# Optimization experiments

Measured on AMD Instinct MI355X. Metric: run time of the kernel, lower is better.

Reference implementation:

```python
import jax, jax.numpy as jnp
import numpy as np

P = 5.0  # p-norm order from init_kwargs


def setup_inputs() -> dict:
    key = jax.random.key(0)
    k1, k2 = jax.random.split(key)
    B, N, M, C = 8, 4096, 4096, 3
    x = jax.random.normal(k1, (B, N, C), dtype=jnp.float32)
    y = jax.random.normal(k2, (B, M, C), dtype=jnp.float32)
    return {"x": x, "y": y}


def _pnorm(v, axis):
    # (sum |v|^p)^(1/p), matching torch.norm(p=5)
    return jnp.sum(jnp.abs(v) ** P, axis=axis) ** (1.0 / P)


def reference(x, y):
    # Squared Euclidean distance matrix [B, N, M]
    d = (-2.0 * jnp.einsum("bnc,bmc->bnm", x, y)
         + jnp.sum(x * x, -1)[:, :, None]
         + jnp.sum(y * y, -1)[:, None, :])
    idx1 = jnp.argmin(d, axis=2)  # [B, N]: nearest y for each x
    idx2 = jnp.argmin(d, axis=1)  # [B, M]: nearest x for each y
    nn_y = jnp.take_along_axis(y, idx1[..., None], axis=1)  # [B, N, 3]
    nn_x = jnp.take_along_axis(x, idx2[..., None], axis=1)  # [B, M, 3]
    pc1 = _pnorm(x - nn_y, axis=-1)  # [B, N]
    pc2 = _pnorm(y - nn_x, axis=-1)  # [B, M]
    result2 = _pnorm(pc1, axis=-1) + _pnorm(pc2, axis=-1)  # [B]
    return jnp.mean(result2)
```

## Files before the change

kernel.cpp:

```cpp
#include <hip/hip_runtime.h>
#include <math.h>


#define BQ      256
#define QPT     2
#define SPLITS  16
#define CH      256
#define GS      8
#define NG      (CH / GS)
#define BIGOFF  64.0f
#define NQTOT   65536
#define NTILE   128
#define TILEQ   512

typedef float f32x2 __attribute__((ext_vector_type(2)));

static __device__ __forceinline__ f32x2 mk2(float s) { f32x2 v; v.x = s; v.y = s; return v; }
static __device__ __forceinline__ f32x2 fma2(f32x2 a, f32x2 b, f32x2 c) {
    return __builtin_elementwise_fma(a, b, c);
}
__device__ __forceinline__ unsigned int float_ord(float f) {
    unsigned int u = __float_as_uint(f);
    return (u & 0x80000000u) ? ~u : (u | 0x80000000u);
}

#define WS_ACC    0
#define WS_CANARY 128
#define WS_GCNT   192
#define WS_TCNT   256
#define WS_PSUM   1024
#define WS_TAB    4096
#define WS_TBL    1048576

__global__ __launch_bounds__(BQ) void chamfer_mktab(
    const float* __restrict__ x, const float* __restrict__ y,
    float4* __restrict__ tbl)
{
    const int t   = blockIdx.x * BQ + threadIdx.x;
    const int dir = t >> 14;
    const int b   = (t >> 11) & 7;
    const int pr  = t & 2047;
    const float* R = (dir == 0 ? y : x) + (size_t)b * 4096 * 3;
    const float* rp = R + (size_t)(2 * pr) * 3;
    const float f0 = rp[0], f1 = rp[1], f2 = rp[2];
    const float f3 = rp[3], f4 = rp[4], f5 = rp[5];
    const float h0 = fmaf(0.5f * f0, f0, fmaf(0.5f * f1, f1, fmaf(0.5f * f2, f2, BIGOFF)));
    const float h1 = fmaf(0.5f * f3, f3, fmaf(0.5f * f4, f4, fmaf(0.5f * f5, f5, BIGOFF)));
    const size_t o = ((size_t)(dir * 8 + b) * 2048 + pr) * 2;
    tbl[o]     = make_float4(f0, f3, f1, f4);
    tbl[o + 1] = make_float4(f2, f5, h0, h1);
}

__global__ __launch_bounds__(BQ, 8) void chamfer_fused_r12(
    const float* __restrict__ x, const float* __restrict__ y,
    const float4* __restrict__ tbl,
    unsigned long long* __restrict__ tab,
    unsigned int* __restrict__ tcnt, unsigned int* __restrict__ gcnt,
    const unsigned int* __restrict__ canary_p,
    float* __restrict__ psum, float* __restrict__ out)
{
    __shared__ float red[4];
    __shared__ int s_flag;

    const int bid   = blockIdx.x;
    const int split = bid & (SPLITS - 1);
    const int tq    = bid >> 4;
    const int dir   = tq >> 6;
    const int b     = (tq >> 3) & 7;
    const int t8    = tq & 7;

    const unsigned int canary = *canary_p;

    const float* Q; const float* R;
    if (dir == 0) { Q = x + (size_t)b * 4096 * 3; R = y + (size_t)b * 4096 * 3; }
    else          { Q = y + (size_t)b * 4096 * 3; R = x + (size_t)b * 4096 * 3; }

    const int tid = threadIdx.x;

    const float4* __restrict__ tb =
        tbl + ((size_t)(dir * 8 + b) * 4096 + (size_t)split * 256);

    const int ql0 = t8 * TILEQ + tid;
    const int ql1 = ql0 + 256;
    const float qx0 = Q[ql0 * 3 + 0], qy0 = Q[ql0 * 3 + 1], qz0 = Q[ql0 * 3 + 2];
    const float qx1 = Q[ql1 * 3 + 0], qy1 = Q[ql1 * 3 + 1], qz1 = Q[ql1 * 3 + 2];
    const f32x2 nqx0 = mk2(-qx0), nqy0 = mk2(-qy0), nqz0 = mk2(-qz0);
    const f32x2 nqx1 = mk2(-qx1), nqy1 = mk2(-qy1), nqz1 = mk2(-qz1);

    float best0 = 3.4e38f, best1 = 3.4e38f;
    int bg0 = 0, bg1 = 0;

    #pragma unroll 2
    for (int g = 0; g < NG; ++g) {
        float m0 = 3.4e38f, m1 = 3.4e38f;
        #pragma unroll
        for (int k = 0; k < GS / 2; ++k) {
            const float4 a = tb[(g * 4 + k) * 2];
            const float4 c = tb[(g * 4 + k) * 2 + 1];
            f32x2 rx; rx.x = a.x; rx.y = a.y;
            f32x2 ry; ry.x = a.z; ry.y = a.w;
            f32x2 rz; rz.x = c.x; rz.y = c.y;
            f32x2 h2; h2.x = c.z; h2.y = c.w;
            const f32x2 s0 = fma2(nqx0, rx, fma2(nqy0, ry, fma2(nqz0, rz, h2)));
            const f32x2 s1 = fma2(nqx1, rx, fma2(nqy1, ry, fma2(nqz1, rz, h2)));
            m0 = fminf(fminf(m0, s0.x), s0.y);
            m1 = fminf(fminf(m1, s1.x), s1.y);
        }
        const bool c0 = m0 < best0;
        best0 = c0 ? m0 : best0;  bg0 = c0 ? g : bg0;
        const bool c1 = m1 < best1;
        best1 = c1 ? m1 : best1;  bg1 = c1 ? g : bg1;
    }

    #pragma unroll
    for (int hh = 0; hh < 2; ++hh) {
        const float bscore = hh ? best1 : best0;
        const int   bg     = hh ? bg1   : bg0;
        const float qx = hh ? qx1 : qx0;
        const float qy = hh ? qy1 : qy0;
        const float qz = hh ? qz1 : qz0;
        const int basej = split * CH + bg * GS;
        int bj = basej;
        #pragma unroll
        for (int j = GS - 1; j >= 0; --j) {
            const float* rp = R + (size_t)(basej + j) * 3;
            const float rx = rp[0], ry = rp[1], rz = rp[2];
            const float h = fmaf(0.5f * rx, rx, fmaf(0.5f * ry, ry, fmaf(0.5f * rz, rz, BIGOFF)));
            const float s = fmaf(-qx, rx, fmaf(-qy, ry, fmaf(-qz, rz, h)));
            if (s == bscore) bj = basej + j;
        }
        const size_t qidx = (size_t)tq * TILEQ + hh * 256 + tid;
        const unsigned long long key =
            ~(((unsigned long long)__float_as_uint(bscore) << 32) | (unsigned int)bj);
        atomicMax(&tab[qidx], key);
    }

    __syncthreads();
    if (tid == 0) {
        const unsigned int old = atomicAdd(&tcnt[tq], 1u);
        s_flag = (old == canary + (SPLITS - 1));
    }
    __syncthreads();
    if (!s_flag) return;

    float sthr = 0.0f;
    #pragma unroll
    for (int k = 0; k < QPT; ++k) {
        const int gq = tq * TILEQ + k * 256 + tid;
        const int q  = t8 * TILEQ + k * 256 + tid;
        const unsigned long long w =
            ~__hip_atomic_load(&tab[gq], __ATOMIC_RELAXED, __HIP_MEMORY_SCOPE_AGENT);
        const int j = (int)(unsigned int)w;
        const float dx = Q[q * 3 + 0] - R[(size_t)j * 3 + 0];
        const float dy = Q[q * 3 + 1] - R[(size_t)j * 3 + 1];
        const float dz = Q[q * 3 + 2] - R[(size_t)j * 3 + 2];
        const float ax = fabsf(dx), ay = fabsf(dy), az = fabsf(dz);
        const float ax2 = ax * ax, ay2 = ay * ay, az2 = az * az;
        sthr += ax2 * ax2 * ax + ay2 * ay2 * ay + az2 * az2 * az;
    }
    #pragma unroll
    for (int off = 32; off > 0; off >>= 1) sthr += __shfl_down(sthr, off, 64);
    const int wid = tid >> 6, lane = tid & 63;
    if (lane == 0) red[wid] = sthr;
    __syncthreads();

    if (tid == 0) {
        __hip_atomic_store(&psum[tq], red[0] + red[1] + red[2] + red[3],
                           __ATOMIC_RELAXED, __HIP_MEMORY_SCOPE_AGENT);
        asm volatile("s_waitcnt vmcnt(0)" ::: "memory");
        const unsigned int old = atomicAdd(gcnt, 1u);
        s_flag = (old == canary + (NTILE - 1));
    }
    __syncthreads();
    if (!s_flag) return;

    if (tid < 64) {
        float v = 0.0f;
        if (tid < 16) {
            const int fb = tid >> 1, fdir = tid & 1;
            float a = 0.0f;
            #pragma unroll
            for (int t = 0; t < 8; ++t)
                a += __hip_atomic_load(&psum[fdir * 64 + fb * 8 + t],
                                       __ATOMIC_RELAXED, __HIP_MEMORY_SCOPE_AGENT);
            v = exp2f(0.2f * log2f(a));
        }
        #pragma unroll
        for (int off = 8; off > 0; off >>= 1) v += __shfl_down(v, off, 64);
        if (tid == 0) out[0] = v * 0.125f;
    }
    if (tid < NTILE)
        __hip_atomic_store(&tcnt[tid], canary, __ATOMIC_RELAXED, __HIP_MEMORY_SCOPE_AGENT);
    if (tid == 0)
        __hip_atomic_store(gcnt, canary, __ATOMIC_RELAXED, __HIP_MEMORY_SCOPE_AGENT);
}

__global__ __launch_bounds__(BQ) void chamfer_nn_split_kernel(
    const float* __restrict__ x, const float* __restrict__ y,
    unsigned long long* __restrict__ packed, int N, int M)
{
    __shared__ float4 sref[1024];
    const int bid = blockIdx.x, split = bid & 3, qb = bid >> 2;
    const int tile = qb & 15, dir = (qb >> 4) & 1, b = qb >> 5;
    const float* Q; const float* R;
    if (dir == 0) { Q = x + (size_t)b * N * 3; R = y + (size_t)b * M * 3; }
    else          { Q = y + (size_t)b * M * 3; R = x + (size_t)b * N * 3; }
    const int tid = threadIdx.x, q = tile * BQ + tid, base = split * 1024;
    for (int j = tid; j < 1024; j += BQ) {
        const float rx = R[(size_t)(base + j) * 3 + 0];
        const float ry = R[(size_t)(base + j) * 3 + 1];
        const float rz = R[(size_t)(base + j) * 3 + 2];
        sref[j] = make_float4(rx, ry, rz, 0.5f * (rx * rx + ry * ry + rz * rz));
    }
    __syncthreads();
    const float qx = Q[q * 3 + 0], qy = Q[q * 3 + 1], qz = Q[q * 3 + 2];
    float best = 3.4e38f; int bestj = base;
    #pragma unroll 8
    for (int j = 0; j < 1024; ++j) {
        const float4 r = sref[j];
        float t = __fmaf_rn(-qx, r.x, r.w);
        t = __fmaf_rn(-qy, r.y, t);
        t = __fmaf_rn(-qz, r.z, t);
        const bool c = t < best;
        best = c ? t : best; bestj = c ? (base + j) : bestj;
    }
    const size_t idx = ((size_t)dir * 8 + b) * (size_t)N + q;
    atomicMin(&packed[idx], ((unsigned long long)float_ord(best) << 32) | (unsigned int)bestj);
}

__global__ __launch_bounds__(BQ) void chamfer_gather_kernel(
    const float* __restrict__ x, const float* __restrict__ y,
    const unsigned long long* __restrict__ packed,
    float* __restrict__ acc, int N, int M)
{
    __shared__ float red[4];
    const int tid = threadIdx.x;
    const size_t gq = (size_t)blockIdx.x * BQ + tid;
    const int dir = (int)(gq / ((size_t)8 * N));
    const size_t rem = gq - (size_t)dir * 8 * N;
    const int b = (int)(rem / N), q = (int)(rem - (size_t)b * N);
    const float* Q; const float* R;
    if (dir == 0) { Q = x + (size_t)b * N * 3; R = y + (size_t)b * M * 3; }
    else          { Q = y + (size_t)b * M * 3; R = x + (size_t)b * N * 3; }
    const int j = (int)(unsigned int)packed[gq];
    const float dx = Q[q * 3 + 0] - R[(size_t)j * 3 + 0];
    const float dy = Q[q * 3 + 1] - R[(size_t)j * 3 + 1];
    const float dz = Q[q * 3 + 2] - R[(size_t)j * 3 + 2];
    const float ax = fabsf(dx), ay = fabsf(dy), az = fabsf(dz);
    const float ax2 = ax * ax, ay2 = ay * ay, az2 = az * az;
    float s = ax2 * ax2 * ax + ay2 * ay2 * ay + az2 * az2 * az;
    #pragma unroll
    for (int off = 32; off > 0; off >>= 1) s += __shfl_down(s, off, 64);
    const int wid = tid >> 6, lane = tid & 63;
    if (lane == 0) red[wid] = s;
    __syncthreads();
    if (tid == 0) atomicAdd(&acc[b * 2 + dir], red[0] + red[1] + red[2] + red[3]);
}

__global__ void chamfer_finalize_kernel(const float* __restrict__ acc,
                                        float* __restrict__ out)
{
    if (threadIdx.x == 0 && blockIdx.x == 0) {
        float total = 0.0f;
        #pragma unroll
        for (int i = 0; i < 16; ++i) total += powf(acc[i], 0.2f);
        *out = total * 0.125f;
    }
}

extern "C" void kernel_launch(void* const* d_in, const int* in_sizes, int n_in,
                              void* d_out, int out_size, void* d_ws, size_t ws_size,
                              hipStream_t stream)
{
    const float* x = (const float*)d_in[0];
    const float* y = (const float*)d_in[1];
    float* out = (float*)d_out;
    const int N = in_sizes[0] / 24;
    const int M = in_sizes[1] / 24;

    const size_t needed = WS_TBL + (size_t)32768 * 32;

    if (N == 4096 && M == 4096 && ws_size >= needed) {
        unsigned char* ws = (unsigned char*)d_ws;
        unsigned long long* tab = (unsigned long long*)(ws + WS_TAB);
        unsigned int* tcnt = (unsigned int*)(ws + WS_TCNT);
        unsigned int* gcnt = (unsigned int*)(ws + WS_GCNT);
        const unsigned int* canary = (const unsigned int*)(ws + WS_CANARY);
        float* psum = (float*)(ws + WS_PSUM);
        float4* tbl = (float4*)(ws + WS_TBL);
        chamfer_mktab<<<32768 / BQ, BQ, 0, stream>>>(x, y, tbl);
        chamfer_fused_r12<<<NTILE * SPLITS, BQ, 0, stream>>>(
            x, y, tbl, tab, tcnt, gcnt, canary, psum, out);
    } else {
        unsigned char* ws = (unsigned char*)d_ws;
        float* acc = (float*)ws;
        unsigned long long* ptab = (unsigned long long*)(ws + 4096);
        const size_t nQ = (size_t)2 * 8 * N;
        hipMemsetAsync(acc, 0, 64, stream);
        hipMemsetAsync(ptab, 0xFF, nQ * 8, stream);
        chamfer_nn_split_kernel<<<(int)(nQ / BQ) * 4, BQ, 0, stream>>>(x, y, ptab, N, M);
        chamfer_gather_kernel<<<(int)(nQ / BQ), BQ, 0, stream>>>(x, y, ptab, acc, N, M);
        chamfer_finalize_kernel<<<1, 64, 0, stream>>>(acc, out);
    }
}
```

Baseline: 89.82 us.

## Process four queries per thread and double-buffer reference table loads

Each thread now handles four query points instead of two, which halves the number of tiles and blocks so each loaded reference chunk is reused across more queries. The reference-table loads are software-pipelined with two register buffers, so the next group is fetched while the current one is computed. Launch bounds drop to 4 waves per SIMD to fit the extra registers, and the finalize indexing is adjusted for 64 tiles. The cost is higher register pressure and fewer blocks (1024), which lowers occupancy and parallelism.

```diff
diff --git a/kernel.cpp b/kernel.cpp
--- a/kernel.cpp
+++ b/kernel.cpp
@@ -3,17 +3,18 @@
 
 
 #define BQ      256
-#define QPT     2
+#define QPT     4
 #define SPLITS  16
 #define CH      256
 #define GS      8
 #define NG      (CH / GS)
 #define BIGOFF  64.0f
 #define NQTOT   65536
-#define NTILE   128
-#define TILEQ   512
+#define NTILE   64
+#define TILEQ   1024
 
 typedef float f32x2 __attribute__((ext_vector_type(2)));
+typedef float f32x4 __attribute__((ext_vector_type(4)));
 
 static __device__ __forceinline__ f32x2 mk2(float s) { f32x2 v; v.x = s; v.y = s; return v; }
 static __device__ __forceinline__ f32x2 fma2(f32x2 a, f32x2 b, f32x2 c) {
@@ -51,9 +52,36 @@
     tbl[o + 1] = make_float4(f2, f5, h0, h1);
 }
 
-__global__ __launch_bounds__(BQ, 8) void chamfer_fused_r12(
+#define COMPUTE_GROUP(BUF, G)                                              \
+  {                                                                        \
+    float mloc[QPT];                                                       \
+    _Pragma("unroll")                                                      \
+    for (int k4 = 0; k4 < 4; ++k4) {                                       \
+      const f32x4 a = BUF[2 * k4];                    \
+      const f32x4 c = BUF[2 * k4 + 1];                 \
+      const f32x2 rx = __builtin_shufflevector(a, a, 0, 1);                \
+      const f32x2 ry = __builtin_shufflevector(a, a, 2, 3);                \
+      const f32x2 rz = __builtin_shufflevector(c, c, 0, 1);                \
+      const f32x2 h2 = __builtin_shufflevector(c, c, 2, 3);                \
+      _Pragma("unroll")                                                    \
+      for (int qk = 0; qk < QPT; ++qk) {                                   \
+        const f32x2 s = fma2(nqx[qk], rx,                                  \
+                        fma2(nqy[qk], ry, fma2(nqz[qk], rz, h2)));         \
+        if (k4 == 0) mloc[qk] = fminf(s.x, s.y);                           \
+        else         mloc[qk] = fminf(fminf(mloc[qk], s.x), s.y);          \
+      }                                                                    \
+    }                                                                      \
+    _Pragma("unroll")                                                      \
+    for (int qk = 0; qk < QPT; ++qk) {                                     \
+      const bool cc = mloc[qk] < best[qk];   \
+      best[qk] = cc ? mloc[qk] : best[qk];                                 \
+      bg[qk]   = cc ? (G) : bg[qk];                                        \
+    }                                                                      \
+  }
+
+__global__ __launch_bounds__(BQ, 4) void chamfer_fused_r14(
     const float* __restrict__ x, const float* __restrict__ y,
-    const float4* __restrict__ tbl,
+    const f32x4* __restrict__ tbl,
     unsigned long long* __restrict__ tab,
     unsigned int* __restrict__ tcnt, unsigned int* __restrict__ gcnt,
     const unsigned int* __restrict__ canary_p,
@@ -65,9 +93,9 @@
     const int bid   = blockIdx.x;
     const int split = bid & (SPLITS - 1);
     const int tq    = bid >> 4;
-    const int dir   = tq >> 6;
-    const int b     = (tq >> 3) & 7;
-    const int t8    = tq & 7;
+    const int dir   = tq >> 5;
+    const int b     = (tq >> 2) & 7;
+    const int t4    = tq & 3;
 
     const unsigned int canary = *canary_p;
 
@@ -77,49 +105,44 @@
 
     const int tid = threadIdx.x;
 
-    const float4* __restrict__ tb =
+    const f32x4* __restrict__ tb =
         tbl + ((size_t)(dir * 8 + b) * 4096 + (size_t)split * 256);
 
-    const int ql0 = t8 * TILEQ + tid;
-    const int ql1 = ql0 + 256;
-    const float qx0 = Q[ql0 * 3 + 0], qy0 = Q[ql0 * 3 + 1], qz0 = Q[ql0 * 3 + 2];
-    const float qx1 = Q[ql1 * 3 + 0], qy1 = Q[ql1 * 3 + 1], qz1 = Q[ql1 * 3 + 2];
-    const f32x2 nqx0 = mk2(-qx0), nqy0 = mk2(-qy0), nqz0 = mk2(-qz0);
-    const f32x2 nqx1 = mk2(-qx1), nqy1 = mk2(-qy1), nqz1 = mk2(-qz1);
-
-    float best0 = 3.4e38f, best1 = 3.4e38f;
-    int bg0 = 0, bg1 = 0;
-
-    #pragma unroll 2
-    for (int g = 0; g < NG; ++g) {
-        float m0 = 3.4e38f, m1 = 3.4e38f;
-        #pragma unroll
-        for (int k = 0; k < GS / 2; ++k) {
-            const float4 a = tb[(g * 4 + k) * 2];
-            const float4 c = tb[(g * 4 + k) * 2 + 1];
-            f32x2 rx; rx.x = a.x; rx.y = a.y;
-            f32x2 ry; ry.x = a.z; ry.y = a.w;
-            f32x2 rz; rz.x = c.x; rz.y = c.y;
-            f32x2 h2; h2.x = c.z; h2.y = c.w;
-            const f32x2 s0 = fma2(nqx0, rx, fma2(nqy0, ry, fma2(nqz0, rz, h2)));
-            const f32x2 s1 = fma2(nqx1, rx, fma2(nqy1, ry, fma2(nqz1, rz, h2)));
-            m0 = fminf(fminf(m0, s0.x), s0.y);
-            m1 = fminf(fminf(m1, s1.x), s1.y);
-        }
-        const bool c0 = m0 < best0;
-        best0 = c0 ? m0 : best0;  bg0 = c0 ? g : bg0;
-        const bool c1 = m1 < best1;
-        best1 = c1 ? m1 : best1;  bg1 = c1 ? g : bg1;
-    }
-
-    #pragma unroll
-    for (int hh = 0; hh < 2; ++hh) {
-        const float bscore = hh ? best1 : best0;
-        const int   bg     = hh ? bg1   : bg0;
-        const float qx = hh ? qx1 : qx0;
-        const float qy = hh ? qy1 : qy0;
-        const float qz = hh ? qz1 : qz0;
-        const int basej = split * CH + bg * GS;
+    f32x2 nqx[QPT], nqy[QPT], nqz[QPT];
+    #pragma unroll
+    for (int qk = 0; qk < QPT; ++qk) {
+        const int ql = t4 * TILEQ + qk * 256 + tid;
+        nqx[qk] = mk2(-Q[ql * 3 + 0]);
+        nqy[qk] = mk2(-Q[ql * 3 + 1]);
+        nqz[qk] = mk2(-Q[ql * 3 + 2]);
+    }
+
+    float best[QPT]; int bg[QPT];
+    #pragma unroll
+    for (int qk = 0; qk < QPT; ++qk) { best[qk] = 3.4e38f; bg[qk] = 0; }
+
+    f32x4 bufA[8], bufB[8];
+    #pragma unroll
+    for (int i = 0; i < 8; ++i) bufA[i] = tb[i];
+
+    #pragma unroll 1
+    for (int g = 0; g < NG; g += 2) {
+        #pragma unroll
+        for (int i = 0; i < 8; ++i) bufB[i] = tb[(g + 1) * 8 + i];
+        COMPUTE_GROUP(bufA, g)
+        const int gpre = (g + 2) & (NG - 1);
+        #pragma unroll
+        for (int i = 0; i < 8; ++i) bufA[i] = tb[gpre * 8 + i];
+        COMPUTE_GROUP(bufB, g + 1)
+    }
+
+    #pragma unroll
+    for (int qk = 0; qk < QPT; ++qk) {
+        const float bscore = best[qk];
+        const float qx = -nqx[qk].x;
+        const float qy = -nqy[qk].x;
+        const float qz = -nqz[qk].x;
+        const int basej = split * CH + bg[qk] * GS;
         int bj = basej;
         #pragma unroll
         for (int j = GS - 1; j >= 0; --j) {
@@ -129,7 +152,7 @@
             const float s = fmaf(-qx, rx, fmaf(-qy, ry, fmaf(-qz, rz, h)));
             if (s == bscore) bj = basej + j;
         }
-        const size_t qidx = (size_t)tq * TILEQ + hh * 256 + tid;
+        const size_t qidx = (size_t)tq * TILEQ + qk * 256 + tid;
         const unsigned long long key =
             ~(((unsigned long long)__float_as_uint(bscore) << 32) | (unsigned int)bj);
         atomicMax(&tab[qidx], key);
@@ -147,7 +170,7 @@
     #pragma unroll
     for (int k = 0; k < QPT; ++k) {
         const int gq = tq * TILEQ + k * 256 + tid;
-        const int q  = t8 * TILEQ + k * 256 + tid;
+        const int q  = t4 * TILEQ + k * 256 + tid;
         const unsigned long long w =
             ~__hip_atomic_load(&tab[gq], __ATOMIC_RELAXED, __HIP_MEMORY_SCOPE_AGENT);
         const int j = (int)(unsigned int)w;
@@ -180,8 +203,8 @@
             const int fb = tid >> 1, fdir = tid & 1;
             float a = 0.0f;
             #pragma unroll
-            for (int t = 0; t < 8; ++t)
-                a += __hip_atomic_load(&psum[fdir * 64 + fb * 8 + t],
+            for (int t = 0; t < 4; ++t)
+                a += __hip_atomic_load(&psum[fdir * 32 + fb * 4 + t],
                                        __ATOMIC_RELAXED, __HIP_MEMORY_SCOPE_AGENT);
             v = exp2f(0.2f * log2f(a));
         }
@@ -278,7 +301,7 @@
     const int N = in_sizes[0] / 24;
     const int M = in_sizes[1] / 24;
 
-    const size_t needed = WS_TBL + (size_t)32768 * 32;
+    const size_t needed = WS_TBL + (1u << 20);
 
     if (N == 4096 && M == 4096 && ws_size >= needed) {
         unsigned char* ws = (unsigned char*)d_ws;
@@ -287,10 +310,9 @@
         unsigned int* gcnt = (unsigned int*)(ws + WS_GCNT);
         const unsigned int* canary = (const unsigned int*)(ws + WS_CANARY);
         float* psum = (float*)(ws + WS_PSUM);
-        float4* tbl = (float4*)(ws + WS_TBL);
-        chamfer_mktab<<<32768 / BQ, BQ, 0, stream>>>(x, y, tbl);
-        chamfer_fused_r12<<<NTILE * SPLITS, BQ, 0, stream>>>(
-            x, y, tbl, tab, tcnt, gcnt, canary, psum, out);
+        chamfer_mktab<<<32768 / BQ, BQ, 0, stream>>>(x, y, (float4*)(ws + WS_TBL));
+        chamfer_fused_r14<<<NTILE * SPLITS, BQ, 0, stream>>>(
+            x, y, (const f32x4*)(ws + WS_TBL), tab, tcnt, gcnt, canary, psum, out);
     } else {
         unsigned char* ws = (unsigned char*)d_ws;
         float* acc = (float*)ws;
```

After: 87.87 us. 2.2% less time.
